# Optimization experiments

Hardware: AMD Instinct MI355X
Metric: run time of the kernel (lower is better)

Reference implementation:

```python
import jax, jax.numpy as jnp
import numpy as np

P = 25          # number of 3x3 positions on a 7x7 board (5x5 grid)
B = 8192        # batch
C_IN = 2        # input planes
DM = 128        # dim_middle
DF = 32         # dim_feature
CMAX = 127.0 / 128.0


def setup_inputs() -> dict:
    key = jax.random.key(0)
    ks = jax.random.split(key, 16)
    s = 0.05
    return {
        "x": jax.random.normal(ks[0], (B, C_IN, 7, 7), dtype=jnp.float32),
        # per-position (25 distinct towers) conv weights, torch layout (out,in,kh,kw)
        "W1": jax.random.normal(ks[1], (P, DM, C_IN, 2, 2), dtype=jnp.float32) * s,
        "b1": jax.random.normal(ks[2], (P, DM), dtype=jnp.float32) * s,
        "W2": jax.random.normal(ks[3], (P, DM, DM, 2, 2), dtype=jnp.float32) * s,
        "b2": jax.random.normal(ks[4], (P, DM), dtype=jnp.float32) * s,
        "W3": jax.random.normal(ks[5], (P, DM, DM), dtype=jnp.float32) * s,   # 1x1 conv
        "b3": jax.random.normal(ks[6], (P, DM), dtype=jnp.float32) * s,
        "W4": jax.random.normal(ks[7], (P, DF, DM), dtype=jnp.float32) * s,   # 1x1 conv, no act
        "b4": jax.random.normal(ks[8], (P, DF), dtype=jnp.float32) * s,
        # NNUE head MLP
        "fc1_w": jax.random.normal(ks[9], (DF, DF), dtype=jnp.float32) * s,
        "fc1_b": jax.random.normal(ks[10], (DF,), dtype=jnp.float32) * s,
        "fc2_w": jax.random.normal(ks[11], (DF, DF), dtype=jnp.float32) * s,
        "fc2_b": jax.random.normal(ks[12], (DF,), dtype=jnp.float32) * s,
        "fc3_w": jax.random.normal(ks[13], (1, DF), dtype=jnp.float32) * s,
        "fc3_b": jax.random.normal(ks[14], (1,), dtype=jnp.float32) * s,
    }


def _tower(x, W1, b1, W2, b2, W3, b3, W4, b4):
    # Gather the 25 3x3 patches -> [P, B, C, 3, 3] (fixed small Python loop over positions)
    patches = jnp.stack([x[:, :, y:y + 3, xx:xx + 3]
                         for y in range(5) for xx in range(5)], axis=0)
    # Conv1: 2x2 kernel on 3x3 -> 2x2 output, per-position weights, + ReLU
    h = jnp.stack([
        jnp.stack([
            jnp.einsum('pbcij,pocij->pbo', patches[..., i:i + 2, j:j + 2], W1)
            for j in range(2)], axis=-1)
        for i in range(2)], axis=-2)                       # [P, B, DM, 2, 2]
    h = jax.nn.relu(h + b1[:, None, :, None, None])
    # Conv2: 2x2 kernel on 2x2 -> 1x1, + ReLU
    h = jax.nn.relu(jnp.einsum('pbcij,pocij->pbo', h, W2) + b2[:, None, :])  # [P, B, DM]
    # Conv3: 1x1, + ReLU
    h = jax.nn.relu(jnp.einsum('pbc,poc->pbo', h, W3) + b3[:, None, :])
    # Conv4: 1x1, no activation, then clamp to [-1, 127/128]
    f = jnp.einsum('pbc,poc->pbo', h, W4) + b4[:, None, :]                   # [P, B, DF]
    f = jnp.clip(f, -1.0, CMAX)
    return f.sum(axis=0)                                    # [B, DF]


def reference(x, W1, b1, W2, b2, W3, b3, W4, b4,
              fc1_w, fc1_b, fc2_w, fc2_b, fc3_w, fc3_b):
    feature = _tower(x, W1, b1, W2, b2, W3, b3, W4, b4)
    v = jnp.clip(feature, 0.0, CMAX)
    # NNUE head: two clipped-ReLU linear layers + scalar output
    v = jnp.clip(v @ fc1_w.T + fc1_b, 0.0, CMAX)
    v = jnp.clip(v @ fc2_w.T + fc2_b, 0.0, CMAX)
    return v @ fc3_w.T + fc3_b                               # [B, 1]
```

## Files before the change

### kernel.cpp

```cpp
#include <hip/hip_runtime.h>
#include <hip/hip_bf16.h>


#define BATCH 8192
#define CMAXF 0.9921875f
#define NGRP 5
#define PPG 5

#define WF_TOTAL 2560000
#define PART_BYTE_OFF 5120000

using bf16x8 = __attribute__((ext_vector_type(8))) short;
using f32x4  = __attribute__((ext_vector_type(4))) float;

__device__ __forceinline__ unsigned short f2bf(float f) {
  union { float f; unsigned u; } v; v.f = f;
  unsigned u = v.u + 0x7fffu + ((v.u >> 16) & 1u);
  return (unsigned short)(u >> 16);
}

__device__ __forceinline__ f32x4 mfma16(bf16x8 a, bf16x8 b, f32x4 c) {
  return __builtin_amdgcn_mfma_f32_16x16x32_bf16(a, b, c, 0, 0, 0);
}

__device__ __forceinline__ void relu_pack2(f32x4 v, unsigned& lo, unsigned& hi) {
  union { __hip_bfloat162 h; unsigned u; } a_, b_;
  a_.h = __float22bfloat162_rn(make_float2(fmaxf(v[0], 0.f), fmaxf(v[1], 0.f)));
  b_.h = __float22bfloat162_rn(make_float2(fmaxf(v[2], 0.f), fmaxf(v[3], 0.f)));
  lo = a_.u; hi = b_.u;
}

__global__ __launch_bounds__(256) void prep_kernel(
    const float* __restrict__ W1, const float* __restrict__ b1,
    const float* __restrict__ W2, const float* __restrict__ W3,
    const float* __restrict__ W4, unsigned short* __restrict__ wf)
{
  int e4 = (blockIdx.x * 256 + threadIdx.x) * 4;
  if (e4 >= WF_TOTAL) return;
  const int j0 = e4 & 7;
  const int l = (e4 >> 3) & 63;
  const int f = (e4 >> 9) & 7;
  const int pq = e4 >> 12;
  const int p = pq / 25, q = pq - p * 25;
  const int g = l >> 4, l15 = l & 15;
  unsigned short vv[4];
#pragma unroll
  for (int i = 0; i < 4; ++i) {
    int j = j0 + i;
    float val = 0.f;
    if (q < 20) {
      int s = q / 5, rem = q - s * 5;
      if (rem == 0) {
        int o = f * 16 + l15;
        int kk = g * 8 + j;
        if (kk < 18) {
          int c = (kk >= 9) ? 1 : 0;
          int rr = kk - c * 9;
          int py = rr / 3, px = rr - py * 3;
          int si = s >> 1, sj = s & 1;
          int di = py - si, dj = px - sj;
          if (di >= 0 && di < 2 && dj >= 0 && dj < 2)
            val = W1[((p * 128 + o) * 2 + c) * 4 + di * 2 + dj];
        } else if (kk == 18) {
          val = b1[p * 128 + o];
        }
      } else {
        int kq = rem - 1;
        int o = f * 16 + l15;
        int c = kq * 32 + ((j >> 2) << 4) + g * 4 + (j & 3);
        val = W2[((p * 128 + o) * 128 + c) * 4 + s];
      }
    } else if (q < 24) {
      int kq = q - 20;
      int o = f * 16 + l15;
      int c = kq * 32 + ((j >> 2) << 4) + g * 4 + (j & 3);
      val = W3[(p * 128 + o) * 128 + c];
    } else {
      int nt = f >> 2, kq = f & 3;
      int o = nt * 16 + l15;
      int c = kq * 32 + ((j >> 2) << 4) + g * 4 + (j & 3);
      val = W4[(p * 32 + o) * 128 + c];
    }
    vv[i] = f2bf(val);
  }
  ushort4 st; st.x = vv[0]; st.y = vv[1]; st.z = vv[2]; st.w = vv[3];
  *(ushort4*)(wf + e4) = st;
}

#define BFRAG(pkm, kq) ({                                        \
  union { unsigned u[4]; bf16x8 v; } _bf;                        \
  _bf.u[0] = pkm[2*(kq)][0];   _bf.u[1] = pkm[2*(kq)][1];        \
  _bf.u[2] = pkm[2*(kq)+1][0]; _bf.u[3] = pkm[2*(kq)+1][1];      \
  _bf.v; })

__global__ __launch_bounds__(64, 2) void tower_kernel(
    const float* __restrict__ x,
    const float* __restrict__ b2v, const float* __restrict__ b3v,
    const float* __restrict__ b4v,
    const unsigned short* __restrict__ wf, float* __restrict__ part)
{
  __shared__ __align__(16) unsigned short xsw[32 * 98];

  const int l = threadIdx.x;
  const int l15 = l & 15;
  const int g = l >> 4;

  int bid = blockIdx.x;
  int lin = (bid & 7) * 160 + (bid >> 3);
  int grp = lin >> 8;
  int btile = lin & 255;
  const int R0 = btile * 32;

  for (int idx = l; idx < 32 * 98; idx += 64)
    xsw[idx] = f2bf(x[(size_t)R0 * 98 + idx]);
  __syncthreads();

  int kbase[8]; int kmode[8];
#pragma unroll
  for (int j = 0; j < 8; ++j) {
    int k = g * 8 + j;
    if (k < 18) {
      int c = (k >= 9) ? 1 : 0;
      int rr = k - c * 9;
      int py = rr / 3, px = rr - (rr / 3) * 3;
      kbase[j] = c * 49 + py * 7 + px;
      kmode[j] = 1;
    } else { kbase[j] = 0; kmode[j] = (k == 18) ? 2 : 0; }
  }

  const f32x4 zf = {0.f, 0.f, 0.f, 0.f};
  f32x4 facc[2][2] = {{zf, zf}, {zf, zf}};

  bf16x8 wA[8], wB[8];

#define PRE(DST, PN, QN)                                                          \
  {                                                                               \
    const unsigned short* s_ = wf + ((size_t)((PN) * 25 + (QN)) * 8) * 512 + l * 8; \
    _Pragma("unroll")                                                             \
    for (int f_ = 0; f_ < 8; ++f_) DST[f_] = *(const bf16x8*)(s_ + f_ * 512);     \
  }

#define L1PH(W)                                                                   \
  {                                                                               \
    __builtin_amdgcn_s_setprio(1);                                                \
    _Pragma("unroll")                                                             \
    for (int t_ = 0; t_ < 8; ++t_) {                                              \
      f32x4 c0_ = mfma16(W[t_], a1x[0], zf);                                      \
      f32x4 c1_ = mfma16(W[t_], a1x[1], zf);                                      \
      relu_pack2(c0_, pk[0][t_][0], pk[0][t_][1]);                                \
      relu_pack2(c1_, pk[1][t_][0], pk[1][t_][1]);                                \
    }                                                                             \
    __builtin_amdgcn_s_setprio(0);                                                \
  }

#define L2PH(W, KQ)                                                               \
  {                                                                               \
    bf16x8 bA_ = BFRAG(pk[0], KQ), bB_ = BFRAG(pk[1], KQ);                        \
    __builtin_amdgcn_s_setprio(1);                                                \
    _Pragma("unroll")                                                             \
    for (int t_ = 0; t_ < 8; ++t_) {                                              \
      acc[t_][0] = mfma16(W[t_], bA_, acc[t_][0]);                                \
      acc[t_][1] = mfma16(W[t_], bB_, acc[t_][1]);                                \
    }                                                                             \
    __builtin_amdgcn_s_setprio(0);                                                \
  }

  PRE(wA, grp * PPG, 0);

#pragma unroll 1
  for (int pp = 0; pp < PPG; ++pp) {
    const int p = grp * PPG + pp;
    const int y0 = p / 5;
    const int x0 = p - y0 * 5;
    const int poff = y0 * 7 + x0;

    bf16x8 a1x[2];
#pragma unroll
    for (int m = 0; m < 2; ++m) {
#pragma unroll
      for (int j = 0; j < 8; ++j) {
        unsigned short v = 0;
        if (kmode[j] == 1) v = xsw[(m * 16 + l15) * 98 + kbase[j] + poff];
        else if (kmode[j] == 2) v = 0x3F80;
        a1x[m][j] = (short)v;
      }
    }

    f32x4 acc[8][2];
#pragma unroll
    for (int t = 0; t < 8; ++t) {
      f32x4 b2 = *(const f32x4*)(b2v + p * 128 + t * 16 + g * 4);
      acc[t][0] = b2; acc[t][1] = b2;
    }

    unsigned pk[2][8][2];

#pragma unroll
    for (int s = 0; s < 4; ++s) {
      if ((s & 1) == 0) { PRE(wB, p, 5 * s + 1); L1PH(wA); }
      else              { PRE(wA, p, 5 * s + 1); L1PH(wB); }
#pragma unroll
      for (int kq = 0; kq < 4; ++kq) {
        if (((5 * s + 1 + kq) & 1) == 0) { PRE(wB, p, 5 * s + 2 + kq); L2PH(wA, kq); }
        else                             { PRE(wA, p, 5 * s + 2 + kq); L2PH(wB, kq); }
      }
    }

#pragma unroll
    for (int t = 0; t < 8; ++t) {
      f32x4 b3 = *(const f32x4*)(b3v + p * 128 + t * 16 + g * 4);
      relu_pack2(acc[t][0], pk[0][t][0], pk[0][t][1]);
      relu_pack2(acc[t][1], pk[1][t][0], pk[1][t][1]);
      acc[t][0] = b3; acc[t][1] = b3;
    }

#pragma unroll
    for (int kq = 0; kq < 4; ++kq) {
      if (((20 + kq) & 1) == 0) { PRE(wB, p, 21 + kq); L2PH(wA, kq); }
      else                      { PRE(wA, p, 21 + kq); L2PH(wB, kq); }
    }

#pragma unroll
    for (int t = 0; t < 8; ++t) {
      relu_pack2(acc[t][0], pk[0][t][0], pk[0][t][1]);
      relu_pack2(acc[t][1], pk[1][t][0], pk[1][t][1]);
    }

    f32x4 c4[2][2];
#pragma unroll
    for (int nt = 0; nt < 2; ++nt) {
      f32x4 b4 = *(const f32x4*)(b4v + p * 32 + nt * 16 + g * 4);
      c4[nt][0] = b4; c4[nt][1] = b4;
    }

    PRE(wB, p + 1, 0);
    {
      __builtin_amdgcn_s_setprio(1);
#pragma unroll
      for (int kq = 0; kq < 4; ++kq) {
        bf16x8 bA_ = BFRAG(pk[0], kq), bB_ = BFRAG(pk[1], kq);
#pragma unroll
        for (int nt = 0; nt < 2; ++nt) {
          c4[nt][0] = mfma16(wA[nt * 4 + kq], bA_, c4[nt][0]);
          c4[nt][1] = mfma16(wA[nt * 4 + kq], bB_, c4[nt][1]);
        }
      }
      __builtin_amdgcn_s_setprio(0);
#pragma unroll
      for (int nt = 0; nt < 2; ++nt) {
#pragma unroll
        for (int m = 0; m < 2; ++m) {
#pragma unroll
          for (int r = 0; r < 4; ++r) {
            float v = c4[nt][m][r];
            v = fminf(fmaxf(v, -1.f), CMAXF);
            facc[m][nt][r] += v;
          }
        }
      }
    }

#pragma unroll
    for (int f = 0; f < 8; ++f) wA[f] = wB[f];
  }
#undef PRE
#undef L1PH
#undef L2PH

#pragma unroll
  for (int m = 0; m < 2; ++m) {
#pragma unroll
    for (int nt = 0; nt < 2; ++nt) {
      *(f32x4*)(part + ((size_t)grp * BATCH + R0 + m * 16 + l15) * 32 + nt * 16 + g * 4)
          = facc[m][nt];
    }
  }
}

__global__ __launch_bounds__(256) void head_kernel(
    const float* __restrict__ part,
    const float* __restrict__ fc1w, const float* __restrict__ fc1b,
    const float* __restrict__ fc2w, const float* __restrict__ fc2b,
    const float* __restrict__ fc3w, const float* __restrict__ fc3b,
    float* __restrict__ out)
{
  const int lane = threadIdx.x & 63;
  const int o = lane & 31;
  const int half = lane >> 5;
  const int wave = threadIdx.x >> 6;
  const int row = blockIdx.x * 8 + wave * 2 + half;

  float feat = 0.f;
#pragma unroll
  for (int gi = 0; gi < NGRP; ++gi)
    feat += part[((size_t)gi * BATCH + row) * 32 + o];
  feat = feat < 0.f ? 0.f : (feat > CMAXF ? CMAXF : feat);

  float a = fc1b[o];
#pragma unroll
  for (int k = 0; k < 32; ++k)
    a += __shfl(feat, k, 32) * fc1w[o * 32 + k];
  a = a < 0.f ? 0.f : (a > CMAXF ? CMAXF : a);

  float b = fc2b[o];
#pragma unroll
  for (int k = 0; k < 32; ++k)
    b += __shfl(a, k, 32) * fc2w[o * 32 + k];
  b = b < 0.f ? 0.f : (b > CMAXF ? CMAXF : b);

  float c = b * fc3w[o];
#pragma unroll
  for (int m = 16; m >= 1; m >>= 1)
    c += __shfl_xor(c, m, 32);
  if (o == 0) out[row] = c + fc3b[0];
}

extern "C" void kernel_launch(void* const* d_in, const int* in_sizes, int n_in,
                              void* d_out, int out_size, void* d_ws, size_t ws_size,
                              hipStream_t stream) {
  const float* x    = (const float*)d_in[0];
  const float* W1   = (const float*)d_in[1];
  const float* b1   = (const float*)d_in[2];
  const float* W2   = (const float*)d_in[3];
  const float* b2   = (const float*)d_in[4];
  const float* W3   = (const float*)d_in[5];
  const float* b3   = (const float*)d_in[6];
  const float* W4   = (const float*)d_in[7];
  const float* b4   = (const float*)d_in[8];
  const float* fc1w = (const float*)d_in[9];
  const float* fc1b = (const float*)d_in[10];
  const float* fc2w = (const float*)d_in[11];
  const float* fc2b = (const float*)d_in[12];
  const float* fc3w = (const float*)d_in[13];
  const float* fc3b = (const float*)d_in[14];
  float* out = (float*)d_out;

  unsigned short* wf = (unsigned short*)d_ws;
  float* part = (float*)((char*)d_ws + PART_BYTE_OFF);

  prep_kernel<<<WF_TOTAL / 1024, 256, 0, stream>>>(W1, b1, W2, W3, W4, wf);
  tower_kernel<<<1280, 64, 0, stream>>>(x, b2, b3, b4, wf, part);
  head_kernel<<<BATCH / 8, 256, 0, stream>>>(part, fc1w, fc1b, fc2w, fc2b, fc3w, fc3b, out);
}
```

Baseline: 86.39 us.

## Split tower work into 4-wave blocks of 16 rows with lockstep weight loads

Each block now has four waves, each handling 16 batch rows instead of one wave handling 32. All four waves stream the same per-position weight fragments, kept in step by s_barrier, so the loads can hit in cache. Per-wave register use drops roughly by half (one M-tile), which allows higher occupancy. In exchange each weight fragment now feeds only one MFMA per wave instead of two, and the barriers add sync overhead.

```diff
diff --git a/kernel.cpp b/kernel.cpp
--- a/kernel.cpp
+++ b/kernel.cpp
@@ -93,27 +93,29 @@
   _bf.u[2] = pkm[2*(kq)+1][0]; _bf.u[3] = pkm[2*(kq)+1][1];      \
   _bf.v; })
 
-__global__ __launch_bounds__(64, 2) void tower_kernel(
+__global__ __launch_bounds__(256, 3) void tower_kernel(
     const float* __restrict__ x,
     const float* __restrict__ b2v, const float* __restrict__ b3v,
     const float* __restrict__ b4v,
     const unsigned short* __restrict__ wf, float* __restrict__ part)
 {
-  __shared__ __align__(16) unsigned short xsw[32 * 98];
-
-  const int l = threadIdx.x;
+  __shared__ __align__(16) unsigned short xs[4][16 * 98];
+
+  const int tid = threadIdx.x;
+  const int l = tid & 63;
+  const int wv = tid >> 6;
   const int l15 = l & 15;
   const int g = l >> 4;
 
   int bid = blockIdx.x;
-  int lin = (bid & 7) * 160 + (bid >> 3);
-  int grp = lin >> 8;
-  int btile = lin & 255;
-  const int R0 = btile * 32;
-
-  for (int idx = l; idx < 32 * 98; idx += 64)
+  int lin = (bid & 7) * 80 + (bid >> 3);
+  int grp = lin / 128;
+  int btile = lin - grp * 128;
+  const int R0 = btile * 64 + wv * 16;
+
+  unsigned short* xsw = xs[wv];
+  for (int idx = l; idx < 16 * 98; idx += 64)
     xsw[idx] = f2bf(x[(size_t)R0 * 98 + idx]);
-  __syncthreads();
 
   int kbase[8]; int kmode[8];
 #pragma unroll
@@ -129,9 +131,11 @@
   }
 
   const f32x4 zf = {0.f, 0.f, 0.f, 0.f};
-  f32x4 facc[2][2] = {{zf, zf}, {zf, zf}};
+  f32x4 facc[2] = {zf, zf};
 
   bf16x8 wA[8], wB[8];
+
+#define BARX() __builtin_amdgcn_s_barrier()
 
 #define PRE(DST, PN, QN)                                                          \
   {                                                                               \
@@ -145,22 +149,19 @@
     __builtin_amdgcn_s_setprio(1);                                                \
     _Pragma("unroll")                                                             \
     for (int t_ = 0; t_ < 8; ++t_) {                                              \
-      f32x4 c0_ = mfma16(W[t_], a1x[0], zf);                                      \
-      f32x4 c1_ = mfma16(W[t_], a1x[1], zf);                                      \
-      relu_pack2(c0_, pk[0][t_][0], pk[0][t_][1]);                                \
-      relu_pack2(c1_, pk[1][t_][0], pk[1][t_][1]);                                \
+      f32x4 c0_ = mfma16(W[t_], a1x, zf);                                         \
+      relu_pack2(c0_, pk[t_][0], pk[t_][1]);                                      \
     }                                                                             \
     __builtin_amdgcn_s_setprio(0);                                                \
   }
 
 #define L2PH(W, KQ)                                                               \
   {                                                                               \
-    bf16x8 bA_ = BFRAG(pk[0], KQ), bB_ = BFRAG(pk[1], KQ);                        \
+    bf16x8 bA_ = BFRAG(pk, KQ);                                                   \
     __builtin_amdgcn_s_setprio(1);                                                \
     _Pragma("unroll")                                                             \
     for (int t_ = 0; t_ < 8; ++t_) {                                              \
-      acc[t_][0] = mfma16(W[t_], bA_, acc[t_][0]);                                \
-      acc[t_][1] = mfma16(W[t_], bB_, acc[t_][1]);                                \
+      acc[t_] = mfma16(W[t_], bA_, acc[t_]);                                      \
     }                                                                             \
     __builtin_amdgcn_s_setprio(0);                                                \
   }
@@ -174,33 +175,30 @@
     const int x0 = p - y0 * 5;
     const int poff = y0 * 7 + x0;
 
-    bf16x8 a1x[2];
-#pragma unroll
-    for (int m = 0; m < 2; ++m) {
-#pragma unroll
-      for (int j = 0; j < 8; ++j) {
-        unsigned short v = 0;
-        if (kmode[j] == 1) v = xsw[(m * 16 + l15) * 98 + kbase[j] + poff];
-        else if (kmode[j] == 2) v = 0x3F80;
-        a1x[m][j] = (short)v;
-      }
-    }
-
-    f32x4 acc[8][2];
-#pragma unroll
-    for (int t = 0; t < 8; ++t) {
-      f32x4 b2 = *(const f32x4*)(b2v + p * 128 + t * 16 + g * 4);
-      acc[t][0] = b2; acc[t][1] = b2;
-    }
-
-    unsigned pk[2][8][2];
+    bf16x8 a1x;
+#pragma unroll
+    for (int j = 0; j < 8; ++j) {
+      unsigned short v = 0;
+      if (kmode[j] == 1) v = xsw[l15 * 98 + kbase[j] + poff];
+      else if (kmode[j] == 2) v = 0x3F80;
+      a1x[j] = (short)v;
+    }
+
+    f32x4 acc[8];
+#pragma unroll
+    for (int t = 0; t < 8; ++t)
+      acc[t] = *(const f32x4*)(b2v + p * 128 + t * 16 + g * 4);
+
+    unsigned pk[8][2];
 
 #pragma unroll
     for (int s = 0; s < 4; ++s) {
+      BARX();
       if ((s & 1) == 0) { PRE(wB, p, 5 * s + 1); L1PH(wA); }
       else              { PRE(wA, p, 5 * s + 1); L1PH(wB); }
 #pragma unroll
       for (int kq = 0; kq < 4; ++kq) {
+        BARX();
         if (((5 * s + 1 + kq) & 1) == 0) { PRE(wB, p, 5 * s + 2 + kq); L2PH(wA, kq); }
         else                             { PRE(wA, p, 5 * s + 2 + kq); L2PH(wB, kq); }
       }
@@ -209,53 +207,45 @@
 #pragma unroll
     for (int t = 0; t < 8; ++t) {
       f32x4 b3 = *(const f32x4*)(b3v + p * 128 + t * 16 + g * 4);
-      relu_pack2(acc[t][0], pk[0][t][0], pk[0][t][1]);
-      relu_pack2(acc[t][1], pk[1][t][0], pk[1][t][1]);
-      acc[t][0] = b3; acc[t][1] = b3;
+      relu_pack2(acc[t], pk[t][0], pk[t][1]);
+      acc[t] = b3;
     }
 
 #pragma unroll
     for (int kq = 0; kq < 4; ++kq) {
+      BARX();
       if (((20 + kq) & 1) == 0) { PRE(wB, p, 21 + kq); L2PH(wA, kq); }
       else                      { PRE(wA, p, 21 + kq); L2PH(wB, kq); }
     }
 
 #pragma unroll
-    for (int t = 0; t < 8; ++t) {
-      relu_pack2(acc[t][0], pk[0][t][0], pk[0][t][1]);
-      relu_pack2(acc[t][1], pk[1][t][0], pk[1][t][1]);
-    }
-
-    f32x4 c4[2][2];
-#pragma unroll
-    for (int nt = 0; nt < 2; ++nt) {
-      f32x4 b4 = *(const f32x4*)(b4v + p * 32 + nt * 16 + g * 4);
-      c4[nt][0] = b4; c4[nt][1] = b4;
-    }
-
+    for (int t = 0; t < 8; ++t)
+      relu_pack2(acc[t], pk[t][0], pk[t][1]);
+
+    f32x4 c4[2];
+#pragma unroll
+    for (int nt = 0; nt < 2; ++nt)
+      c4[nt] = *(const f32x4*)(b4v + p * 32 + nt * 16 + g * 4);
+
+    BARX();
     PRE(wB, p + 1, 0);
     {
       __builtin_amdgcn_s_setprio(1);
 #pragma unroll
       for (int kq = 0; kq < 4; ++kq) {
-        bf16x8 bA_ = BFRAG(pk[0], kq), bB_ = BFRAG(pk[1], kq);
-#pragma unroll
-        for (int nt = 0; nt < 2; ++nt) {
-          c4[nt][0] = mfma16(wA[nt * 4 + kq], bA_, c4[nt][0]);
-          c4[nt][1] = mfma16(wA[nt * 4 + kq], bB_, c4[nt][1]);
-        }
+        bf16x8 bA_ = BFRAG(pk, kq);
+#pragma unroll
+        for (int nt = 0; nt < 2; ++nt)
+          c4[nt] = mfma16(wA[nt * 4 + kq], bA_, c4[nt]);
       }
       __builtin_amdgcn_s_setprio(0);
 #pragma unroll
       for (int nt = 0; nt < 2; ++nt) {
 #pragma unroll
-        for (int m = 0; m < 2; ++m) {
-#pragma unroll
-          for (int r = 0; r < 4; ++r) {
-            float v = c4[nt][m][r];
-            v = fminf(fmaxf(v, -1.f), CMAXF);
-            facc[m][nt][r] += v;
-          }
+        for (int r = 0; r < 4; ++r) {
+          float v = c4[nt][r];
+          v = fminf(fmaxf(v, -1.f), CMAXF);
+          facc[nt][r] += v;
         }
       }
     }
@@ -266,14 +256,12 @@
 #undef PRE
 #undef L1PH
 #undef L2PH
-
-#pragma unroll
-  for (int m = 0; m < 2; ++m) {
-#pragma unroll
-    for (int nt = 0; nt < 2; ++nt) {
-      *(f32x4*)(part + ((size_t)grp * BATCH + R0 + m * 16 + l15) * 32 + nt * 16 + g * 4)
-          = facc[m][nt];
-    }
+#undef BARX
+
+#pragma unroll
+  for (int nt = 0; nt < 2; ++nt) {
+    *(f32x4*)(part + ((size_t)grp * BATCH + R0 + l15) * 32 + nt * 16 + g * 4)
+        = facc[nt];
   }
 }
 
@@ -339,6 +327,6 @@
   float* part = (float*)((char*)d_ws + PART_BYTE_OFF);
 
   prep_kernel<<<WF_TOTAL / 1024, 256, 0, stream>>>(W1, b1, W2, W3, W4, wf);
-  tower_kernel<<<1280, 64, 0, stream>>>(x, b2, b3, b4, wf, part);
+  tower_kernel<<<640, 256, 0, stream>>>(x, b2, b3, b4, wf, part);
   head_kernel<<<BATCH / 8, 256, 0, stream>>>(part, fc1w, fc1b, fc2w, fc2b, fc3w, fc3b, out);
 }
```

After: 127.2 us. 1.47x slower.

## Triple-buffer weight fragment prefetch to deepen global-load pipelining

Applied to the files above, without the earlier changes.

Replaces the double-buffered weight fragment registers with three rotating buffers, so each weight chunk is prefetched two MFMA phases ahead instead of one. The aim is to hide global/L2 load latency behind more matrix work. The extra 64 VGPRs per lane force the occupancy hint down from 2 to 1 wave per SIMD, which gives up latency hiding between waves in exchange for deeper latency hiding within a wave.

```diff
diff --git a/kernel.cpp b/kernel.cpp
--- a/kernel.cpp
+++ b/kernel.cpp
@@ -93,7 +93,7 @@
   _bf.u[2] = pkm[2*(kq)+1][0]; _bf.u[3] = pkm[2*(kq)+1][1];      \
   _bf.v; })
 
-__global__ __launch_bounds__(64, 2) void tower_kernel(
+__global__ __launch_bounds__(64, 1) void tower_kernel(
     const float* __restrict__ x,
     const float* __restrict__ b2v, const float* __restrict__ b3v,
     const float* __restrict__ b4v,
@@ -131,7 +131,7 @@
   const f32x4 zf = {0.f, 0.f, 0.f, 0.f};
   f32x4 facc[2][2] = {{zf, zf}, {zf, zf}};
 
-  bf16x8 wA[8], wB[8];
+  bf16x8 wX[8], wY[8], wZ[8];
 
 #define PRE(DST, PN, QN)                                                          \
   {                                                                               \
@@ -165,7 +165,8 @@
     __builtin_amdgcn_s_setprio(0);                                                \
   }
 
-  PRE(wA, grp * PPG, 0);
+  PRE(wX, grp * PPG, 0);
+  PRE(wY, grp * PPG, 1);
 
 #pragma unroll 1
   for (int pp = 0; pp < PPG; ++pp) {
@@ -195,16 +196,26 @@
 
     unsigned pk[2][8][2];
 
-#pragma unroll
-    for (int s = 0; s < 4; ++s) {
-      if ((s & 1) == 0) { PRE(wB, p, 5 * s + 1); L1PH(wA); }
-      else              { PRE(wA, p, 5 * s + 1); L1PH(wB); }
-#pragma unroll
-      for (int kq = 0; kq < 4; ++kq) {
-        if (((5 * s + 1 + kq) & 1) == 0) { PRE(wB, p, 5 * s + 2 + kq); L2PH(wA, kq); }
-        else                             { PRE(wA, p, 5 * s + 2 + kq); L2PH(wB, kq); }
-      }
-    }
+    PRE(wZ, p, 2);  L1PH(wX);
+    PRE(wX, p, 3);  L2PH(wY, 0);
+    PRE(wY, p, 4);  L2PH(wZ, 1);
+    PRE(wZ, p, 5);  L2PH(wX, 2);
+    PRE(wX, p, 6);  L2PH(wY, 3);
+    PRE(wY, p, 7);  L1PH(wZ);
+    PRE(wZ, p, 8);  L2PH(wX, 0);
+    PRE(wX, p, 9);  L2PH(wY, 1);
+    PRE(wY, p, 10); L2PH(wZ, 2);
+    PRE(wZ, p, 11); L2PH(wX, 3);
+    PRE(wX, p, 12); L1PH(wY);
+    PRE(wY, p, 13); L2PH(wZ, 0);
+    PRE(wZ, p, 14); L2PH(wX, 1);
+    PRE(wX, p, 15); L2PH(wY, 2);
+    PRE(wY, p, 16); L2PH(wZ, 3);
+    PRE(wZ, p, 17); L1PH(wX);
+    PRE(wX, p, 18); L2PH(wY, 0);
+    PRE(wY, p, 19); L2PH(wZ, 1);
+    PRE(wZ, p, 20); L2PH(wX, 2);
+    PRE(wX, p, 21); L2PH(wY, 3);
 
 #pragma unroll
     for (int t = 0; t < 8; ++t) {
@@ -214,11 +225,10 @@
       acc[t][0] = b3; acc[t][1] = b3;
     }
 
-#pragma unroll
-    for (int kq = 0; kq < 4; ++kq) {
-      if (((20 + kq) & 1) == 0) { PRE(wB, p, 21 + kq); L2PH(wA, kq); }
-      else                      { PRE(wA, p, 21 + kq); L2PH(wB, kq); }
-    }
+    PRE(wY, p, 22);     L2PH(wZ, 0);
+    PRE(wZ, p, 23);     L2PH(wX, 1);
+    PRE(wX, p, 24);     L2PH(wY, 2);
+    PRE(wY, p + 1, 0);  L2PH(wZ, 3);
 
 #pragma unroll
     for (int t = 0; t < 8; ++t) {
@@ -233,7 +243,7 @@
       c4[nt][0] = b4; c4[nt][1] = b4;
     }
 
-    PRE(wB, p + 1, 0);
+    PRE(wZ, p + 1, 1);
     {
       __builtin_amdgcn_s_setprio(1);
 #pragma unroll
@@ -241,8 +251,8 @@
         bf16x8 bA_ = BFRAG(pk[0], kq), bB_ = BFRAG(pk[1], kq);
 #pragma unroll
         for (int nt = 0; nt < 2; ++nt) {
-          c4[nt][0] = mfma16(wA[nt * 4 + kq], bA_, c4[nt][0]);
-          c4[nt][1] = mfma16(wA[nt * 4 + kq], bB_, c4[nt][1]);
+          c4[nt][0] = mfma16(wX[nt * 4 + kq], bA_, c4[nt][0]);
+          c4[nt][1] = mfma16(wX[nt * 4 + kq], bB_, c4[nt][1]);
         }
       }
       __builtin_amdgcn_s_setprio(0);
@@ -261,7 +271,7 @@
     }
 
 #pragma unroll
-    for (int f = 0; f < 8; ++f) wA[f] = wB[f];
+    for (int f = 0; f < 8; ++f) { wX[f] = wY[f]; wY[f] = wZ[f]; }
   }
 #undef PRE
 #undef L1PH
```

Measured after the change: 109.0 us. 26.1% more time.

## Split tower work to one position per block and reduce partials in head

Applied to the files above, without the earlier changes.

The tower kernel now assigns a single board position per block (6400 single-wave blocks) instead of five positions per block, and raises the occupancy hint to 4 waves per SIMD. Each block writes a clamped per-position partial, so the head kernel sums 25 partials instead of 5. The aim is more parallelism and better latency hiding. The cost is loading and converting the x tile to bf16 five times as often, and larger partial-buffer traffic in both kernels. The tighter register budget could also cause spills.

```diff
diff --git a/kernel.cpp b/kernel.cpp
--- a/kernel.cpp
+++ b/kernel.cpp
@@ -4,8 +4,7 @@
 
 #define BATCH 8192
 #define CMAXF 0.9921875f
-#define NGRP 5
-#define PPG 5
+#define NPOS 25
 
 #define WF_TOTAL 2560000
 #define PART_BYTE_OFF 5120000
@@ -93,7 +92,7 @@
   _bf.u[2] = pkm[2*(kq)+1][0]; _bf.u[3] = pkm[2*(kq)+1][1];      \
   _bf.v; })
 
-__global__ __launch_bounds__(64, 2) void tower_kernel(
+__global__ __launch_bounds__(64, 4) void tower_kernel(
     const float* __restrict__ x,
     const float* __restrict__ b2v, const float* __restrict__ b3v,
     const float* __restrict__ b4v,
@@ -106,10 +105,21 @@
   const int g = l >> 4;
 
   int bid = blockIdx.x;
-  int lin = (bid & 7) * 160 + (bid >> 3);
-  int grp = lin >> 8;
-  int btile = lin & 255;
+  int lin = (bid & 7) * 800 + (bid >> 3);
+  int btile = lin / 25;
+  const int p = lin - btile * 25;
   const int R0 = btile * 32;
+
+  bf16x8 wA[8], wB[8];
+
+#define PRE(DST, QN)                                                              \
+  {                                                                               \
+    const unsigned short* s_ = wf + ((size_t)(p * 25 + (QN)) * 8) * 512 + l * 8;  \
+    _Pragma("unroll")                                                             \
+    for (int f_ = 0; f_ < 8; ++f_) DST[f_] = *(const bf16x8*)(s_ + f_ * 512);     \
+  }
+
+  PRE(wA, 0);
 
   for (int idx = l; idx < 32 * 98; idx += 64)
     xsw[idx] = f2bf(x[(size_t)R0 * 98 + idx]);
@@ -129,16 +139,30 @@
   }
 
   const f32x4 zf = {0.f, 0.f, 0.f, 0.f};
-  f32x4 facc[2][2] = {{zf, zf}, {zf, zf}};
-
-  bf16x8 wA[8], wB[8];
-
-#define PRE(DST, PN, QN)                                                          \
-  {                                                                               \
-    const unsigned short* s_ = wf + ((size_t)((PN) * 25 + (QN)) * 8) * 512 + l * 8; \
-    _Pragma("unroll")                                                             \
-    for (int f_ = 0; f_ < 8; ++f_) DST[f_] = *(const bf16x8*)(s_ + f_ * 512);     \
-  }
+  const int y0 = p / 5;
+  const int x0 = p - y0 * 5;
+  const int poff = y0 * 7 + x0;
+
+  bf16x8 a1x[2];
+#pragma unroll
+  for (int m = 0; m < 2; ++m) {
+#pragma unroll
+    for (int j = 0; j < 8; ++j) {
+      unsigned short v = 0;
+      if (kmode[j] == 1) v = xsw[(m * 16 + l15) * 98 + kbase[j] + poff];
+      else if (kmode[j] == 2) v = 0x3F80;
+      a1x[m][j] = (short)v;
+    }
+  }
+
+  f32x4 acc[8][2];
+#pragma unroll
+  for (int t = 0; t < 8; ++t) {
+    f32x4 b2 = *(const f32x4*)(b2v + p * 128 + t * 16 + g * 4);
+    acc[t][0] = b2; acc[t][1] = b2;
+  }
+
+  unsigned pk[2][8][2];
 
 #define L1PH(W)                                                                   \
   {                                                                               \
@@ -165,103 +189,65 @@
     __builtin_amdgcn_s_setprio(0);                                                \
   }
 
-  PRE(wA, grp * PPG, 0);
-
-#pragma unroll 1
-  for (int pp = 0; pp < PPG; ++pp) {
-    const int p = grp * PPG + pp;
-    const int y0 = p / 5;
-    const int x0 = p - y0 * 5;
-    const int poff = y0 * 7 + x0;
-
-    bf16x8 a1x[2];
-#pragma unroll
-    for (int m = 0; m < 2; ++m) {
-#pragma unroll
-      for (int j = 0; j < 8; ++j) {
-        unsigned short v = 0;
-        if (kmode[j] == 1) v = xsw[(m * 16 + l15) * 98 + kbase[j] + poff];
-        else if (kmode[j] == 2) v = 0x3F80;
-        a1x[m][j] = (short)v;
+  PRE(wB, 1);  L1PH(wA);
+  PRE(wA, 2);  L2PH(wB, 0);
+  PRE(wB, 3);  L2PH(wA, 1);
+  PRE(wA, 4);  L2PH(wB, 2);
+  PRE(wB, 5);  L2PH(wA, 3);
+  PRE(wA, 6);  L1PH(wB);
+  PRE(wB, 7);  L2PH(wA, 0);
+  PRE(wA, 8);  L2PH(wB, 1);
+  PRE(wB, 9);  L2PH(wA, 2);
+  PRE(wA, 10); L2PH(wB, 3);
+  PRE(wB, 11); L1PH(wA);
+  PRE(wA, 12); L2PH(wB, 0);
+  PRE(wB, 13); L2PH(wA, 1);
+  PRE(wA, 14); L2PH(wB, 2);
+  PRE(wB, 15); L2PH(wA, 3);
+  PRE(wA, 16); L1PH(wB);
+  PRE(wB, 17); L2PH(wA, 0);
+  PRE(wA, 18); L2PH(wB, 1);
+  PRE(wB, 19); L2PH(wA, 2);
+  PRE(wA, 20); L2PH(wB, 3);
+
+#pragma unroll
+  for (int t = 0; t < 8; ++t) {
+    f32x4 b3 = *(const f32x4*)(b3v + p * 128 + t * 16 + g * 4);
+    relu_pack2(acc[t][0], pk[0][t][0], pk[0][t][1]);
+    relu_pack2(acc[t][1], pk[1][t][0], pk[1][t][1]);
+    acc[t][0] = b3; acc[t][1] = b3;
+  }
+
+  PRE(wB, 21); L2PH(wA, 0);
+  PRE(wA, 22); L2PH(wB, 1);
+  PRE(wB, 23); L2PH(wA, 2);
+  PRE(wA, 24); L2PH(wB, 3);
+
+#pragma unroll
+  for (int t = 0; t < 8; ++t) {
+    relu_pack2(acc[t][0], pk[0][t][0], pk[0][t][1]);
+    relu_pack2(acc[t][1], pk[1][t][0], pk[1][t][1]);
+  }
+
+  f32x4 c4[2][2];
+#pragma unroll
+  for (int nt = 0; nt < 2; ++nt) {
+    f32x4 b4 = *(const f32x4*)(b4v + p * 32 + nt * 16 + g * 4);
+    c4[nt][0] = b4; c4[nt][1] = b4;
+  }
+
+  {
+    __builtin_amdgcn_s_setprio(1);
+#pragma unroll
+    for (int kq = 0; kq < 4; ++kq) {
+      bf16x8 bA_ = BFRAG(pk[0], kq), bB_ = BFRAG(pk[1], kq);
+#pragma unroll
+      for (int nt = 0; nt < 2; ++nt) {
+        c4[nt][0] = mfma16(wA[nt * 4 + kq], bA_, c4[nt][0]);
+        c4[nt][1] = mfma16(wA[nt * 4 + kq], bB_, c4[nt][1]);
       }
     }
-
-    f32x4 acc[8][2];
-#pragma unroll
-    for (int t = 0; t < 8; ++t) {
-      f32x4 b2 = *(const f32x4*)(b2v + p * 128 + t * 16 + g * 4);
-      acc[t][0] = b2; acc[t][1] = b2;
-    }
-
-    unsigned pk[2][8][2];
-
-#pragma unroll
-    for (int s = 0; s < 4; ++s) {
-      if ((s & 1) == 0) { PRE(wB, p, 5 * s + 1); L1PH(wA); }
-      else              { PRE(wA, p, 5 * s + 1); L1PH(wB); }
-#pragma unroll
-      for (int kq = 0; kq < 4; ++kq) {
-        if (((5 * s + 1 + kq) & 1) == 0) { PRE(wB, p, 5 * s + 2 + kq); L2PH(wA, kq); }
-        else                             { PRE(wA, p, 5 * s + 2 + kq); L2PH(wB, kq); }
-      }
-    }
-
-#pragma unroll
-    for (int t = 0; t < 8; ++t) {
-      f32x4 b3 = *(const f32x4*)(b3v + p * 128 + t * 16 + g * 4);
-      relu_pack2(acc[t][0], pk[0][t][0], pk[0][t][1]);
-      relu_pack2(acc[t][1], pk[1][t][0], pk[1][t][1]);
-      acc[t][0] = b3; acc[t][1] = b3;
-    }
-
-#pragma unroll
-    for (int kq = 0; kq < 4; ++kq) {
-      if (((20 + kq) & 1) == 0) { PRE(wB, p, 21 + kq); L2PH(wA, kq); }
-      else                      { PRE(wA, p, 21 + kq); L2PH(wB, kq); }
-    }
-
-#pragma unroll
-    for (int t = 0; t < 8; ++t) {
-      relu_pack2(acc[t][0], pk[0][t][0], pk[0][t][1]);
-      relu_pack2(acc[t][1], pk[1][t][0], pk[1][t][1]);
-    }
-
-    f32x4 c4[2][2];
-#pragma unroll
-    for (int nt = 0; nt < 2; ++nt) {
-      f32x4 b4 = *(const f32x4*)(b4v + p * 32 + nt * 16 + g * 4);
-      c4[nt][0] = b4; c4[nt][1] = b4;
-    }
-
-    PRE(wB, p + 1, 0);
-    {
-      __builtin_amdgcn_s_setprio(1);
-#pragma unroll
-      for (int kq = 0; kq < 4; ++kq) {
-        bf16x8 bA_ = BFRAG(pk[0], kq), bB_ = BFRAG(pk[1], kq);
-#pragma unroll
-        for (int nt = 0; nt < 2; ++nt) {
-          c4[nt][0] = mfma16(wA[nt * 4 + kq], bA_, c4[nt][0]);
-          c4[nt][1] = mfma16(wA[nt * 4 + kq], bB_, c4[nt][1]);
-        }
-      }
-      __builtin_amdgcn_s_setprio(0);
-#pragma unroll
-      for (int nt = 0; nt < 2; ++nt) {
-#pragma unroll
-        for (int m = 0; m < 2; ++m) {
-#pragma unroll
-          for (int r = 0; r < 4; ++r) {
-            float v = c4[nt][m][r];
-            v = fminf(fmaxf(v, -1.f), CMAXF);
-            facc[m][nt][r] += v;
-          }
-        }
-      }
-    }
-
-#pragma unroll
-    for (int f = 0; f < 8; ++f) wA[f] = wB[f];
+    __builtin_amdgcn_s_setprio(0);
   }
 #undef PRE
 #undef L1PH
@@ -271,8 +257,11 @@
   for (int m = 0; m < 2; ++m) {
 #pragma unroll
     for (int nt = 0; nt < 2; ++nt) {
-      *(f32x4*)(part + ((size_t)grp * BATCH + R0 + m * 16 + l15) * 32 + nt * 16 + g * 4)
-          = facc[m][nt];
+      f32x4 v;
+#pragma unroll
+      for (int r = 0; r < 4; ++r)
+        v[r] = fminf(fmaxf(c4[nt][m][r], -1.f), CMAXF);
+      *(f32x4*)(part + ((size_t)p * BATCH + R0 + m * 16 + l15) * 32 + nt * 16 + g * 4) = v;
     }
   }
 }
@@ -292,7 +281,7 @@
 
   float feat = 0.f;
 #pragma unroll
-  for (int gi = 0; gi < NGRP; ++gi)
+  for (int gi = 0; gi < NPOS; ++gi)
     feat += part[((size_t)gi * BATCH + row) * 32 + o];
   feat = feat < 0.f ? 0.f : (feat > CMAXF ? CMAXF : feat);
 
@@ -339,6 +328,6 @@
   float* part = (float*)((char*)d_ws + PART_BYTE_OFF);
 
   prep_kernel<<<WF_TOTAL / 1024, 256, 0, stream>>>(W1, b1, W2, W3, W4, wf);
-  tower_kernel<<<1280, 64, 0, stream>>>(x, b2, b3, b4, wf, part);
+  tower_kernel<<<6400, 64, 0, stream>>>(x, b2, b3, b4, wf, part);
   head_kernel<<<BATCH / 8, 256, 0, stream>>>(part, fc1w, fc1b, fc2w, fc2b, fc3w, fc3b, out);
 }
```

Measured after the change: 331.2 us. 3.83x slower.
